# Optimization experiments

Hardware: AMD Instinct MI355X
Metric: run time of the kernel (lower is better)

The kernel has to match this reference:

```python
import jax, jax.numpy as jnp
import numpy as np

BETA = 0.1
IGNORE_INDEX = -100

def setup_inputs() -> dict:
    key = jax.random.key(0)
    k1, k2, k3, k4, k5 = jax.random.split(key, 5)
    B, T, H, V = 4, 256, 2048, 64000
    x = jax.random.normal(k1, (B, T, H), dtype=jnp.float32)
    ref_x = jax.random.normal(k2, (B, T, H), dtype=jnp.float32)
    y = jax.random.randint(k3, (B, T), 0, V, dtype=jnp.int64)
    # lm-head weights (policy and frozen reference), no bias
    W = jax.random.normal(k4, (V, H), dtype=jnp.float32) * 0.02
    ref_W = jax.random.normal(k5, (V, H), dtype=jnp.float32) * 0.02
    return {"x": x, "ref_x": ref_x, "y": y, "W": W, "ref_W": ref_W}

def _seq_logps(inp, w, y):
    # inp: (B,T,H), w: (V,H), y: (B,T) -> per-sequence average token logp (B,)
    logits = jnp.einsum('bth,vh->btv', inp, w)          # (B,T,V)
    lsm = jax.nn.log_softmax(logits, axis=-1)
    mask = (y != IGNORE_INDEX)
    y_safe = jnp.where(mask, y, 0)
    per_tok = jnp.take_along_axis(lsm, y_safe[..., None], axis=-1)[..., 0]  # (B,T)
    return (per_tok * mask).sum(-1) / mask.sum(-1)

def reference(x, ref_x, y, W, ref_W):
    B = x.shape[0]
    half = B // 2  # first half chosen, second half rejected
    policy_logps = _seq_logps(x, W, y)
    ref_logps = _seq_logps(ref_x, ref_W, y)
    pc, pr = policy_logps[:half], policy_logps[half:]
    rc, rr = ref_logps[:half], ref_logps[half:]
    chosen_logratios = pc - rc
    rejected_logratios = pr - rr
    chosen_rewards = BETA * chosen_logratios
    rejected_rewards = BETA * rejected_logratios
    logits_diff = BETA * (chosen_logratios - rejected_logratios)
    losses = -jax.nn.log_sigmoid(logits_diff)
    loss = losses.mean()
    return loss, chosen_rewards, rejected_rewards
```

## Files before the change

### kernel.cpp

```cpp
#include <hip/hip_runtime.h>
#include <stdint.h>

#define Bdim 4
#define Tdim 256
#define Hdim 2048
#define Vdim 64000
#define MROWS (Bdim * Tdim)
#define NTILES (Vdim / 128)
#define BETA 0.1f
#define IGNORE_INDEX (-100)

typedef __bf16 bf16x8 __attribute__((ext_vector_type(8)));
typedef float floatx4 __attribute__((ext_vector_type(4)));

__device__ __forceinline__ unsigned int f2bf(float f) {
  unsigned int u = __float_as_uint(f);
  return (u + 0x7FFFu + ((u >> 16) & 1u)) >> 16;
}

__global__ void cast_kernel(const float* __restrict__ src,
                            unsigned short* __restrict__ dst, long long n) {
  long long i = ((long long)blockIdx.x * blockDim.x + threadIdx.x) * 8;
  if (i + 8 <= n) {
    float4 f0 = *(const float4*)(src + i);
    float4 f1 = *(const float4*)(src + i + 4);
    uint4 o;
    o.x = f2bf(f0.x) | (f2bf(f0.y) << 16);
    o.y = f2bf(f0.z) | (f2bf(f0.w) << 16);
    o.z = f2bf(f1.x) | (f2bf(f1.y) << 16);
    o.w = f2bf(f1.z) | (f2bf(f1.w) << 16);
    *(uint4*)(dst + i) = o;
  }
}

__device__ __forceinline__ void async_load16(const unsigned short* g,
                                             unsigned short* l) {
  __builtin_amdgcn_global_load_lds(
      (const __attribute__((address_space(1))) void*)g,
      (__attribute__((address_space(3))) void*)l, 16, 0, 0);
}

__global__ void __launch_bounds__(256)
gemm_lse_kernel(const unsigned short* __restrict__ A,
                const unsigned short* __restrict__ Wb,
                const int* __restrict__ y,
                float* __restrict__ partials,
                float* __restrict__ tgt) {
  __shared__ unsigned short sA[128 * 32];
  __shared__ unsigned short sB[128 * 32];
  __shared__ float sRM[2][128];
  __shared__ float sRS[2][128];

  const int tid = threadIdx.x;
  const int lane = tid & 63;
  const int wave = tid >> 6;
  const int wm = wave >> 1;
  const int wn = wave & 1;
  const int lr = lane & 15;
  const int kq = lane >> 4;

  const int m0 = blockIdx.x * 128;
  const int n0 = blockIdx.y * 128;

  floatx4 acc[4][4];
#pragma unroll
  for (int i = 0; i < 4; ++i)
#pragma unroll
    for (int j = 0; j < 4; ++j) acc[i][j] = (floatx4){0.f, 0.f, 0.f, 0.f};

  for (int k0 = 0; k0 < Hdim; k0 += 32) {
#pragma unroll
    for (int h = 0; h < 2; ++h) {
      int c = tid + h * 256;
      int row = c >> 2;
      int kc = (c & 3) << 3;
      async_load16(A + (size_t)(m0 + row) * Hdim + k0 + kc, &sA[row * 32 + kc]);
      async_load16(Wb + (size_t)(n0 + row) * Hdim + k0 + kc, &sB[row * 32 + kc]);
    }
    __syncthreads();

    bf16x8 af[4], bfv[4];
#pragma unroll
    for (int i = 0; i < 4; ++i)
      af[i] = *(const bf16x8*)&sA[(wm * 64 + i * 16 + lr) * 32 + kq * 8];
#pragma unroll
    for (int j = 0; j < 4; ++j)
      bfv[j] = *(const bf16x8*)&sB[(wn * 64 + j * 16 + lr) * 32 + kq * 8];

#pragma unroll
    for (int i = 0; i < 4; ++i)
#pragma unroll
      for (int j = 0; j < 4; ++j)
        acc[i][j] = __builtin_amdgcn_mfma_f32_16x16x32_bf16(af[i], bfv[j],
                                                            acc[i][j], 0, 0, 0);
    __syncthreads();
  }

#pragma unroll
  for (int mi = 0; mi < 4; ++mi) {
#pragma unroll
    for (int rg = 0; rg < 4; ++rg) {
      float v0 = acc[mi][0][rg], v1 = acc[mi][1][rg];
      float v2 = acc[mi][2][rg], v3 = acc[mi][3][rg];
      float mx = fmaxf(fmaxf(v0, v1), fmaxf(v2, v3));
#pragma unroll
      for (int d = 1; d < 16; d <<= 1) mx = fmaxf(mx, __shfl_xor(mx, d));
      float sm = expf(v0 - mx) + expf(v1 - mx) + expf(v2 - mx) + expf(v3 - mx);
#pragma unroll
      for (int d = 1; d < 16; d <<= 1) sm += __shfl_xor(sm, d);

      int row_l = wm * 64 + mi * 16 + kq * 4 + rg;
      if (lr == 0) {
        sRM[wn][row_l] = mx;
        sRS[wn][row_l] = sm;
      }

      int row_g = m0 + row_l;
      int tcol = y[row_g];
      int lc = tcol - (n0 + wn * 64);
      if (lc >= 0 && lc < 64 && (lc & 15) == lr) {
        int ni = lc >> 4;
        float tv = (ni == 0) ? acc[mi][0][rg]
                 : (ni == 1) ? acc[mi][1][rg]
                 : (ni == 2) ? acc[mi][2][rg]
                             : acc[mi][3][rg];
        tgt[row_g] = tv;
      }
    }
  }
  __syncthreads();

  if (tid < 128) {
    float ma = sRM[0][tid], mb2 = sRM[1][tid];
    float M = fmaxf(ma, mb2);
    float S = sRS[0][tid] * expf(ma - M) + sRS[1][tid] * expf(mb2 - M);
    *(float2*)&partials[((size_t)(m0 + tid) * NTILES + blockIdx.y) * 2] =
        make_float2(M, S);
  }
}

__global__ void combine_kernel(const float* __restrict__ partials,
                               const float* __restrict__ tgt,
                               const int* __restrict__ y,
                               float* __restrict__ tlogp) {
  int lane = threadIdx.x & 63;
  int row = blockIdx.x * (blockDim.x >> 6) + (threadIdx.x >> 6);
  float m = -__builtin_inff();
  float s = 0.f;
  for (int t = lane; t < NTILES; t += 64) {
    float2 p = *(const float2*)&partials[((size_t)row * NTILES + t) * 2];
    float nm = fmaxf(m, p.x);
    s = s * expf(m - nm) + p.y * expf(p.x - nm);
    m = nm;
  }
#pragma unroll
  for (int d = 1; d < 64; d <<= 1) {
    float om = __shfl_xor(m, d);
    float os = __shfl_xor(s, d);
    float nm = fmaxf(m, om);
    s = s * expf(m - nm) + os * expf(om - nm);
    m = nm;
  }
  if (lane == 0) {
    int yv = y[row];
    float lse = m + logf(s);
    tlogp[row] = (yv != IGNORE_INDEX) ? (tgt[row] - lse) : 0.f;
  }
}

__global__ void final_kernel(const float* __restrict__ tlogp,
                             const int* __restrict__ y,
                             float* __restrict__ out) {
  __shared__ float redv[4], redk[4];
  __shared__ float seq[2][4];
  int tid = threadIdx.x, lane = tid & 63, w = tid >> 6;
  for (int m = 0; m < 2; ++m) {
    for (int b = 0; b < 4; ++b) {
      int row = b * Tdim + tid;
      float v = tlogp[m * MROWS + row];
      float k = (y[row] != IGNORE_INDEX) ? 1.f : 0.f;
#pragma unroll
      for (int d = 1; d < 64; d <<= 1) {
        v += __shfl_xor(v, d);
        k += __shfl_xor(k, d);
      }
      if (lane == 0) { redv[w] = v; redk[w] = k; }
      __syncthreads();
      if (tid == 0)
        seq[m][b] = (redv[0] + redv[1] + redv[2] + redv[3]) /
                    (redk[0] + redk[1] + redk[2] + redk[3]);
      __syncthreads();
    }
  }
  if (tid == 0) {
    float cl0 = seq[0][0] - seq[1][0];
    float cl1 = seq[0][1] - seq[1][1];
    float rl0 = seq[0][2] - seq[1][2];
    float rl1 = seq[0][3] - seq[1][3];
    float d0 = BETA * (cl0 - rl0);
    float d1 = BETA * (cl1 - rl1);
    float l0 = d0 > 0.f ? log1pf(expf(-d0)) : (-d0 + log1pf(expf(d0)));
    float l1 = d1 > 0.f ? log1pf(expf(-d1)) : (-d1 + log1pf(expf(d1)));
    out[0] = 0.5f * (l0 + l1);
    out[1] = BETA * cl0;
    out[2] = BETA * cl1;
    out[3] = BETA * rl0;
    out[4] = BETA * rl1;
  }
}

extern "C" void kernel_launch(void* const* d_in, const int* in_sizes, int n_in,
                              void* d_out, int out_size, void* d_ws,
                              size_t ws_size, hipStream_t stream) {
  const float* x     = (const float*)d_in[0];
  const float* ref_x = (const float*)d_in[1];
  const int*   y     = (const int*)d_in[2];
  const float* W     = (const float*)d_in[3];
  const float* ref_W = (const float*)d_in[4];
  float* out = (float*)d_out;

  char* ws = (char*)d_ws;
  unsigned short* Wb = (unsigned short*)ws;
  unsigned short* xb = (unsigned short*)(ws + 262144000LL);
  float* partials    = (float*)(ws + 262144000LL + 4194304LL);
  float* tgt         = (float*)(ws + 262144000LL + 4194304LL + 4096000LL);
  float* tlogp       = (float*)(ws + 262144000LL + 4194304LL + 4096000LL + 4096LL);

  const long long nW = (long long)Vdim * Hdim;
  const long long nX = (long long)MROWS * Hdim;

  for (int model = 0; model < 2; ++model) {
    const float* xm = model ? ref_x : x;
    const float* Wm = model ? ref_W : W;
    cast_kernel<<<(unsigned)(nW / (8 * 256)), 256, 0, stream>>>(Wm, Wb, nW);
    cast_kernel<<<(unsigned)(nX / (8 * 256)), 256, 0, stream>>>(xm, xb, nX);
    gemm_lse_kernel<<<dim3(MROWS / 128, NTILES), 256, 0, stream>>>(
        xb, Wb, y, partials, tgt);
    combine_kernel<<<MROWS / 4, 256, 0, stream>>>(partials, tgt, y,
                                                  tlogp + model * MROWS);
  }
  final_kernel<<<1, 256, 0, stream>>>(tlogp, y, out);
}
```

Baseline: 2.084 ms.

## Double-buffer LDS tiles, swizzle LDS layout, and remap blocks for XCD locality

The GEMM main loop now uses two LDS buffers, so the async global-to-LDS loads for the next K-step are issued before computing the current one. Completion is tracked with explicit vmcnt waits and raw barriers in place of two __syncthreads per step. The LDS layout gets an XOR swizzle on the 16-byte slot index to cut bank conflicts on fragment reads. The 2D grid becomes a 1D grid whose index remap groups the 8 M-blocks of one vocab tile so they share W reads in cache, likely by XCD. In exchange LDS use doubles and correctness now depends on the hand-counted vmcnt values.

Result: faster. 1.883 ms (-9.6%).

```diff
diff --git a/kernel.cpp b/kernel.cpp
--- a/kernel.cpp
+++ b/kernel.cpp
@@ -7,6 +7,7 @@
 #define Vdim 64000
 #define MROWS (Bdim * Tdim)
 #define NTILES (Vdim / 128)
+#define NKSTEPS (Hdim / 32)
 #define BETA 0.1f
 #define IGNORE_INDEX (-100)
 
@@ -46,8 +47,8 @@
                 const int* __restrict__ y,
                 float* __restrict__ partials,
                 float* __restrict__ tgt) {
-  __shared__ unsigned short sA[128 * 32];
-  __shared__ unsigned short sB[128 * 32];
+  __shared__ unsigned short sA[2][128 * 32];
+  __shared__ unsigned short sB[2][128 * 32];
   __shared__ float sRM[2][128];
   __shared__ float sRS[2][128];
 
@@ -59,8 +60,30 @@
   const int lr = lane & 15;
   const int kq = lane >> 4;
 
-  const int m0 = blockIdx.x * 128;
-  const int n0 = blockIdx.y * 128;
+  const int f = blockIdx.x;
+  const int L = (f & 7) * 500 + (f >> 3);
+  const int nb = L >> 3;
+  const int mb = L & 7;
+  const int m0 = mb * 128;
+  const int n0 = nb * 128;
+
+  const int c0 = tid;
+  const int c1 = tid + 256;
+  const int r0 = c0 >> 2, r1 = c1 >> 2;
+  const int s0 = (c0 & 3) ^ ((r0 >> 1) & 3);
+  const int s1 = (c1 & 3) ^ ((r1 >> 1) & 3);
+  const unsigned short* gA0 = A + (size_t)(m0 + r0) * Hdim + s0 * 8;
+  const unsigned short* gA1 = A + (size_t)(m0 + r1) * Hdim + s1 * 8;
+  const unsigned short* gB0 = Wb + (size_t)(n0 + r0) * Hdim + s0 * 8;
+  const unsigned short* gB1 = Wb + (size_t)(n0 + r1) * Hdim + s1 * 8;
+  unsigned short* lA0base = &sA[0][c0 * 8];
+  unsigned short* lA1base = &sA[0][c1 * 8];
+  unsigned short* lB0base = &sB[0][c0 * 8];
+  unsigned short* lB1base = &sB[0][c1 * 8];
+
+  const int slotE = (kq ^ ((lr >> 1) & 3)) * 8;
+  const int offA = (wm * 64 + lr) * 32 + slotE;
+  const int offB = (wn * 64 + lr) * 32 + slotE;
 
   floatx4 acc[4][4];
 #pragma unroll
@@ -68,32 +91,47 @@
 #pragma unroll
     for (int j = 0; j < 4; ++j) acc[i][j] = (floatx4){0.f, 0.f, 0.f, 0.f};
 
-  for (int k0 = 0; k0 < Hdim; k0 += 32) {
-#pragma unroll
-    for (int h = 0; h < 2; ++h) {
-      int c = tid + h * 256;
-      int row = c >> 2;
-      int kc = (c & 3) << 3;
-      async_load16(A + (size_t)(m0 + row) * Hdim + k0 + kc, &sA[row * 32 + kc]);
-      async_load16(Wb + (size_t)(n0 + row) * Hdim + k0 + kc, &sB[row * 32 + kc]);
+  auto stage = [&](int buf, int koff) {
+    const int lo = buf * (128 * 32);
+    async_load16(gA0 + koff, lA0base + lo);
+    async_load16(gA1 + koff, lA1base + lo);
+    async_load16(gB0 + koff, lB0base + lo);
+    async_load16(gB1 + koff, lB1base + lo);
+  };
+
+  stage(0, 0);
+
+  for (int kt = 0; kt < NKSTEPS; ++kt) {
+    const int cur = kt & 1;
+    if (kt + 1 < NKSTEPS) {
+      stage(cur ^ 1, (kt + 1) * 32);
+      asm volatile("s_waitcnt vmcnt(4)" ::: "memory");
+    } else {
+      asm volatile("s_waitcnt vmcnt(0)" ::: "memory");
     }
-    __syncthreads();
-
-    bf16x8 af[4], bfv[4];
+    __builtin_amdgcn_s_barrier();
+    asm volatile("" ::: "memory");
+
+    const unsigned short* bufA = &sA[cur][0];
+    const unsigned short* bufB = &sB[cur][0];
+    bf16x8 af[4], bv[4];
 #pragma unroll
     for (int i = 0; i < 4; ++i)
-      af[i] = *(const bf16x8*)&sA[(wm * 64 + i * 16 + lr) * 32 + kq * 8];
+      af[i] = *(const bf16x8*)&bufA[offA + i * 512];
 #pragma unroll
     for (int j = 0; j < 4; ++j)
-      bfv[j] = *(const bf16x8*)&sB[(wn * 64 + j * 16 + lr) * 32 + kq * 8];
+      bv[j] = *(const bf16x8*)&bufB[offB + j * 512];
 
 #pragma unroll
     for (int i = 0; i < 4; ++i)
 #pragma unroll
       for (int j = 0; j < 4; ++j)
-        acc[i][j] = __builtin_amdgcn_mfma_f32_16x16x32_bf16(af[i], bfv[j],
+        acc[i][j] = __builtin_amdgcn_mfma_f32_16x16x32_bf16(af[i], bv[j],
                                                             acc[i][j], 0, 0, 0);
-    __syncthreads();
+
+    asm volatile("s_waitcnt lgkmcnt(0)" ::: "memory");
+    __builtin_amdgcn_s_barrier();
+    asm volatile("" ::: "memory");
   }
 
 #pragma unroll
@@ -134,7 +172,7 @@
     float ma = sRM[0][tid], mb2 = sRM[1][tid];
     float M = fmaxf(ma, mb2);
     float S = sRS[0][tid] * expf(ma - M) + sRS[1][tid] * expf(mb2 - M);
-    *(float2*)&partials[((size_t)(m0 + tid) * NTILES + blockIdx.y) * 2] =
+    *(float2*)&partials[((size_t)(m0 + tid) * NTILES + nb) * 2] =
         make_float2(M, S);
   }
 }
@@ -234,7 +272,7 @@
     const float* Wm = model ? ref_W : W;
     cast_kernel<<<(unsigned)(nW / (8 * 256)), 256, 0, stream>>>(Wm, Wb, nW);
     cast_kernel<<<(unsigned)(nX / (8 * 256)), 256, 0, stream>>>(xm, xb, nX);
-    gemm_lse_kernel<<<dim3(MROWS / 128, NTILES), 256, 0, stream>>>(
+    gemm_lse_kernel<<<MROWS / 128 * NTILES, 256, 0, stream>>>(
         xb, Wb, y, partials, tgt);
     combine_kernel<<<MROWS / 4, 256, 0, stream>>>(partials, tgt, y,
                                                   tlogp + model * MROWS);
```
